# Kernel tuning notes

Measured on AMD Instinct MI355X. Metric: run time of the kernel, lower is better.

The kernel has to match this reference:

```python
import jax, jax.numpy as jnp
import numpy as np

SEQ, B, H, NP, HN = 2048, 2, 2048, 16, 128
SCALE = 1.0 / 11.313708498984761  # 1/sqrt(128), hardcoded in the source baddbmm


def setup_inputs() -> dict:
    key = jax.random.key(0)
    k1, k2, k3 = jax.random.split(key, 3)
    return {
        "hidden_states": jax.random.normal(k1, (SEQ, B, H), dtype=jnp.float32),
        "w_qkv": jax.random.normal(k2, (3 * H, H), dtype=jnp.float32) * 0.02,
        "w_out": jax.random.normal(k3, (H, H), dtype=jnp.float32) * 0.02,
    }


def reference(hidden_states, w_qkv, w_out):
    s, b, h = hidden_states.shape
    # QKV projection (column-parallel linear, no bias): [s, b, 3h]
    qkv = hidden_states @ w_qkv.T
    # [s, b, np, 3*hn] then split (num_query_groups == num_heads)
    qkv = qkv.reshape(s, b, NP, 3 * HN)
    q, k, v = qkv[..., :HN], qkv[..., HN:2 * HN], qkv[..., 2 * HN:]
    # baddbmm QK^T with alpha = 1/sqrt(128): scores [b, np, sq, sk]
    scores = jnp.einsum("sbnh,tbnh->bnst", q, k) * SCALE
    # scale_t == 1 then plain softmax (fallback path; no mask applied)
    prob = jax.nn.softmax(scores, axis=-1)
    # context: bmm(prob, V) -> [sq, b, np, hn] -> [sq, b, h]
    ctx = jnp.einsum("bnst,tbnh->sbnh", prob, v).reshape(s, b, h)
    # row-parallel output linear (no bias)
    return ctx @ w_out.T
```

## Files before the change

kernel.cpp:

```cpp
#include <hip/hip_runtime.h>
#include <stdint.h>

#define SEQ 2048
#define BATCH 2
#define HID 2048
#define NHEADS 16
#define HDIM 128
#define QKV_LD 6144
#define SCALE_F 0.08838834764831845f
#define LOG2E_F 1.4426950408889634f

typedef unsigned short u16;
using bf16x8 = __attribute__((ext_vector_type(8))) short;
using f32x4  = __attribute__((ext_vector_type(4))) float;

__device__ inline u16 f2bf(float f) {
  union { float f; uint32_t u; } c; c.f = f;
  uint32_t u = c.u;
  uint32_t r = (u + 0x7fffu + ((u >> 16) & 1u)) >> 16;
  return (u16)r;
}

__device__ inline void gl_lds16(const u16* g, u16* l) {
  __builtin_amdgcn_global_load_lds((const __attribute__((address_space(1))) void*)g,
                                   (__attribute__((address_space(3))) void*)l,
                                   16, 0, 0);
}

__global__ void cvt_all(const float* __restrict__ hs, const float* __restrict__ wqkv,
                        const float* __restrict__ wout, u16* __restrict__ ws_out) {
  int i = blockIdx.x * blockDim.x + threadIdx.x;
  const float* src;
  int j;
  float sc = 1.0f;
  if (i < 2097152) { src = hs; j = i; }
  else if (i < 5242880) {
    j = i - 2097152; src = wqkv;
    const int f = j >> 9;
    if ((f % 384) < 128) sc = SCALE_F;
  } else { j = i - 5242880; src = wout; }
  float4 v = ((const float4*)src)[j];
  ushort4 o;
  o.x = f2bf(v.x * sc); o.y = f2bf(v.y * sc); o.z = f2bf(v.z * sc); o.w = f2bf(v.w * sc);
  ((ushort4*)ws_out)[i] = o;
}

template<int MODE>
__global__ __launch_bounds__(256)
void gemm_bt(const u16* __restrict__ A, const u16* __restrict__ Bw,
             void* __restrict__ Cout, u16* __restrict__ vt, int M, int N, int K) {
  __shared__ __align__(16) u16 As[128 * 64];
  __shared__ __align__(16) u16 Bs[128 * 64];
  const int bm = blockIdx.x, bn = blockIdx.y;
  const int tid = threadIdx.x;
  const int wave = tid >> 6, lane = tid & 63;
  const int quad = lane >> 4, l16 = lane & 15;
  const int wm = (wave >> 1) * 64, wn = (wave & 1) * 64;
  f32x4 acc[4][4] = {};

  const u16* Ablk = A + (size_t)(bm * 128) * K;
  const u16* Bblk = Bw + (size_t)(bn * 128) * K;

  for (int k0 = 0; k0 < K; k0 += 64) {
    __syncthreads();
    #pragma unroll
    for (int p = 0; p < 4; ++p) {
      int j = p * 256 + tid;
      int r = j >> 3, cs = j & 7, c = cs ^ (r & 7);
      gl_lds16(Ablk + (size_t)r * K + k0 + c * 8, As + (p * 256 + wave * 64) * 8);
      gl_lds16(Bblk + (size_t)r * K + k0 + c * 8, Bs + (p * 256 + wave * 64) * 8);
    }
    __syncthreads();
    #pragma unroll
    for (int ks = 0; ks < 2; ++ks) {
      bf16x8 af[4], bfr[4];
      #pragma unroll
      for (int mt = 0; mt < 4; ++mt) {
        int row = wm + mt * 16 + l16;
        int cc = (ks * 4 + quad) ^ (row & 7);
        af[mt] = *(const bf16x8*)&As[(row * 8 + cc) * 8];
      }
      #pragma unroll
      for (int nt = 0; nt < 4; ++nt) {
        int row = wn + nt * 16 + l16;
        int cc = (ks * 4 + quad) ^ (row & 7);
        bfr[nt] = *(const bf16x8*)&Bs[(row * 8 + cc) * 8];
      }
      #pragma unroll
      for (int mt = 0; mt < 4; ++mt)
        #pragma unroll
        for (int nt = 0; nt < 4; ++nt)
          acc[mt][nt] = __builtin_amdgcn_mfma_f32_16x16x32_bf16(af[mt], bfr[nt], acc[mt][nt], 0, 0, 0);
    }
  }

  if (MODE == 1 && (bn % 3) == 2) {
    const int h = bn / 3;
    u16* vt0 = vt + ((size_t)h * HDIM) * SEQ;
    u16* vt1 = vt + ((size_t)(NHEADS + h) * HDIM) * SEQ;
    #pragma unroll
    for (int mt = 0; mt < 4; ++mt)
      #pragma unroll
      for (int nt = 0; nt < 4; ++nt) {
        const int hd = wn + nt * 16 + l16;
        const int s0 = (bm * 128 + wm + mt * 16 + quad * 4) >> 1;
        uint32_t w0 = (uint32_t)f2bf(acc[mt][nt][0]) | ((uint32_t)f2bf(acc[mt][nt][2]) << 16);
        uint32_t w1 = (uint32_t)f2bf(acc[mt][nt][1]) | ((uint32_t)f2bf(acc[mt][nt][3]) << 16);
        *(uint32_t*)&vt0[(size_t)hd * SEQ + s0] = w0;
        *(uint32_t*)&vt1[(size_t)hd * SEQ + s0] = w1;
      }
    return;
  }

  #pragma unroll
  for (int mt = 0; mt < 4; ++mt)
    #pragma unroll
    for (int nt = 0; nt < 4; ++nt)
      #pragma unroll
      for (int r = 0; r < 4; ++r) {
        int row = bm * 128 + wm + mt * 16 + quad * 4 + r;
        int col = bn * 128 + wn + nt * 16 + l16;
        float v = acc[mt][nt][r];
        if (MODE == 1) ((u16*)Cout)[(size_t)row * N + col] = f2bf(v);
        else           ((float*)Cout)[(size_t)row * N + col] = v;
      }
}

__global__ __launch_bounds__(512, 2)
void attn(const u16* __restrict__ qkv, const u16* __restrict__ vt_g, u16* __restrict__ ctx) {
  const int qt = blockIdx.x, head = blockIdx.y, b = blockIdx.z;
  const int q0 = qt * 256;
  __shared__ __align__(16) u16 Ks[2][64 * 128];
  __shared__ __align__(16) u16 Vt[2][144 * 64];
  __shared__ __align__(16) u16 PsT[256 * 64];
  const int tid = threadIdx.x;
  const int wave = tid >> 6, lane = tid & 63;
  const int quad = lane >> 4, l16 = lane & 15;

  const u16* qkv_bh = qkv + (size_t)b * QKV_LD + head * 384;
  const u16* vt = vt_g + (size_t)(b * NHEADS + head) * HDIM * SEQ;

  if (tid < 128) {
    const int row = 128 + (tid >> 3), c = tid & 7;
    const u16 v = (row == 128) ? (u16)0x3F80 : (u16)0;
    ushort4 q4; q4.x = v; q4.y = v; q4.z = v; q4.w = v;
    #pragma unroll
    for (int bb = 0; bb < 2; ++bb) {
      *(ushort4*)&Vt[bb][(row * 8 + c) * 8] = q4;
      *(ushort4*)&Vt[bb][(row * 8 + c) * 8 + 4] = q4;
    }
  }

  bf16x8 qf[2][4];
  #pragma unroll
  for (int h = 0; h < 4; ++h) {
    __syncthreads();
    #pragma unroll
    for (int p = 0; p < 2; ++p) {
      int j = p * 512 + tid;
      int r = j >> 4, cs = j & 15, c = cs ^ (r & 7);
      gl_lds16(qkv_bh + (size_t)(q0 + h * 64 + r) * (BATCH * QKV_LD) + c * 8,
               Ks[0] + (p * 512 + wave * 64) * 8);
    }
    __syncthreads();
    if ((wave >> 1) == h) {
      #pragma unroll
      for (int nt = 0; nt < 2; ++nt)
        #pragma unroll
        for (int ks = 0; ks < 4; ++ks) {
          int row = (wave & 1) * 32 + nt * 16 + l16;
          int cc = (ks * 4 + quad) ^ (row & 7);
          qf[nt][ks] = *(const bf16x8*)&Ks[0][(row * 16 + cc) * 8];
        }
    }
  }

  auto stageKV = [&](int kt, int bb) {
    #pragma unroll
    for (int p = 0; p < 2; ++p) {
      int j = p * 512 + tid;
      int r = j >> 4, cs = j & 15, c = cs ^ (r & 7);
      gl_lds16(qkv_bh + (size_t)(kt + r) * (BATCH * QKV_LD) + 128 + c * 8,
               Ks[bb] + (p * 512 + wave * 64) * 8);
    }
    #pragma unroll
    for (int p = 0; p < 2; ++p) {
      int j = p * 512 + tid;
      int hd = j >> 3, cs = j & 7, c = cs ^ (hd & 7);
      gl_lds16(vt + (size_t)hd * SEQ + kt + c * 8,
               Vt[bb] + (p * 512 + wave * 64) * 8);
    }
  };

  f32x4 ot[9][2] = {};

  __syncthreads();
  stageKV(0, 0);
  __syncthreads();

  for (int it = 0; it < SEQ / 64; ++it) {
    const int cur = it & 1;
    if (it + 1 < SEQ / 64) stageKV((it + 1) * 64, cur ^ 1);
    const u16* Kb = Ks[cur];
    const u16* Vb = Vt[cur];

    f32x4 st[4][2] = {};
    #pragma unroll
    for (int ks = 0; ks < 4; ++ks) {
      bf16x8 kf[4];
      #pragma unroll
      for (int mt = 0; mt < 4; ++mt) {
        int key = mt * 16 + l16;
        int cc = (ks * 4 + quad) ^ (key & 7);
        kf[mt] = *(const bf16x8*)&Kb[(key * 16 + cc) * 8];
      }
      __builtin_amdgcn_s_setprio(1);
      #pragma unroll
      for (int mt = 0; mt < 4; ++mt)
        #pragma unroll
        for (int nt = 0; nt < 2; ++nt)
          st[mt][nt] = __builtin_amdgcn_mfma_f32_16x16x32_bf16(kf[mt], qf[nt][ks], st[mt][nt], 0, 0, 0);
      __builtin_amdgcn_s_setprio(0);
    }

    #pragma unroll
    for (int mt = 0; mt < 4; ++mt)
      #pragma unroll
      for (int nt = 0; nt < 2; ++nt) {
        ushort4 pk;
        union { float f; uint32_t u; } cv;
        cv.f = __builtin_amdgcn_exp2f(st[mt][nt][0] * LOG2E_F); pk.x = (u16)(cv.u >> 16);
        cv.f = __builtin_amdgcn_exp2f(st[mt][nt][1] * LOG2E_F); pk.y = (u16)(cv.u >> 16);
        cv.f = __builtin_amdgcn_exp2f(st[mt][nt][2] * LOG2E_F); pk.z = (u16)(cv.u >> 16);
        cv.f = __builtin_amdgcn_exp2f(st[mt][nt][3] * LOG2E_F); pk.w = (u16)(cv.u >> 16);
        const int q = wave * 32 + nt * 16 + l16;
        const int kc = mt * 2 + (quad >> 1);
        *(ushort4*)&PsT[q * 64 + ((kc ^ (l16 & 7)) * 8 + (quad & 1) * 4)] = pk;
      }

    #pragma unroll
    for (int ks = 0; ks < 2; ++ks) {
      bf16x8 pf[2], vf[9];
      #pragma unroll
      for (int nt = 0; nt < 2; ++nt) {
        const int q = wave * 32 + nt * 16 + l16;
        const int cc = (ks * 4 + quad) ^ (l16 & 7);
        pf[nt] = *(const bf16x8*)&PsT[q * 64 + cc * 8];
      }
      #pragma unroll
      for (int mt = 0; mt < 9; ++mt) {
        const int hd = mt * 16 + l16;
        const int cc = (ks * 4 + quad) ^ (hd & 7);
        vf[mt] = *(const bf16x8*)&Vb[(hd * 8 + cc) * 8];
      }
      __builtin_amdgcn_s_setprio(1);
      #pragma unroll
      for (int mt = 0; mt < 9; ++mt)
        #pragma unroll
        for (int nt = 0; nt < 2; ++nt)
          ot[mt][nt] = __builtin_amdgcn_mfma_f32_16x16x32_bf16(vf[mt], pf[nt], ot[mt][nt], 0, 0, 0);
      __builtin_amdgcn_s_setprio(0);
    }

    __syncthreads();
  }

  #pragma unroll
  for (int nt = 0; nt < 2; ++nt) {
    const float lv = __shfl(ot[8][nt][0], l16);
    const float inv_l = 1.0f / lv;
    const int s = q0 + wave * 32 + nt * 16 + l16;
    u16* dst = ctx + ((size_t)s * BATCH + b) * HID + head * HDIM;
    #pragma unroll
    for (int mt = 0; mt < 8; ++mt) {
      ushort4 w;
      w.x = f2bf(ot[mt][nt][0] * inv_l);
      w.y = f2bf(ot[mt][nt][1] * inv_l);
      w.z = f2bf(ot[mt][nt][2] * inv_l);
      w.w = f2bf(ot[mt][nt][3] * inv_l);
      *(ushort4*)&dst[mt * 16 + quad * 4] = w;
    }
  }
}

extern "C" void kernel_launch(void* const* d_in, const int* in_sizes, int n_in,
                              void* d_out, int out_size, void* d_ws, size_t ws_size,
                              hipStream_t stream) {
  const float* hs   = (const float*)d_in[0];
  const float* wqkv = (const float*)d_in[1];
  const float* wout = (const float*)d_in[2];
  float* out = (float*)d_out;
  char* ws = (char*)d_ws;

  u16* hs_bf   = (u16*)(ws);
  u16* wqkv_bf = (u16*)(ws + 16777216);
  u16* wout_bf = (u16*)(ws + 41943040);
  u16* qkv_bf  = (u16*)(ws + 50331648);
  u16* vt_bf   = (u16*)(ws + 100663296);
  u16* ctx_bf  = hs_bf;

  cvt_all<<<24576, 256, 0, stream>>>(hs, wqkv, wout, (u16*)ws);

  gemm_bt<1><<<dim3(32, 48), 256, 0, stream>>>(hs_bf, wqkv_bf, qkv_bf, vt_bf, 4096, 6144, 2048);

  attn<<<dim3(8, NHEADS, BATCH), 512, 0, stream>>>(qkv_bf, vt_bf, ctx_bf);

  gemm_bt<0><<<dim3(32, 16), 256, 0, stream>>>(ctx_bf, wout_bf, out, nullptr, 4096, 2048, 2048);
}
```

Baseline: 365.1 us.

## Split output GEMM into 128x64 tiles and compute softmax denominator with VALU sums

The output projection gets its own kernel with 128x64 tiles, launching 1024 blocks instead of 512 so more CUs are kept busy on the 4096x2048 GEMM. In attention, the extra ones-row MFMA tile that produced the softmax row sum is removed. The denominator is instead accumulated from the bf16-rounded probabilities in registers and reduced with cross-lane shuffles. This cuts one ninth of the PV MFMAs and some LDS, in exchange for extra VALU adds and lower data reuse in the smaller output GEMM tiles.

```diff
diff --git a/kernel.cpp b/kernel.cpp
--- a/kernel.cpp
+++ b/kernel.cpp
@@ -45,10 +45,9 @@
   ((ushort4*)ws_out)[i] = o;
 }
 
-template<int MODE>
 __global__ __launch_bounds__(256)
 void gemm_bt(const u16* __restrict__ A, const u16* __restrict__ Bw,
-             void* __restrict__ Cout, u16* __restrict__ vt, int M, int N, int K) {
+             u16* __restrict__ Cout, u16* __restrict__ vt, int M, int N, int K) {
   __shared__ __align__(16) u16 As[128 * 64];
   __shared__ __align__(16) u16 Bs[128 * 64];
   const int bm = blockIdx.x, bn = blockIdx.y;
@@ -94,7 +93,7 @@
     }
   }
 
-  if (MODE == 1 && (bn % 3) == 2) {
+  if ((bn % 3) == 2) {
     const int h = bn / 3;
     u16* vt0 = vt + ((size_t)h * HDIM) * SEQ;
     u16* vt1 = vt + ((size_t)(NHEADS + h) * HDIM) * SEQ;
@@ -120,9 +119,72 @@
       for (int r = 0; r < 4; ++r) {
         int row = bm * 128 + wm + mt * 16 + quad * 4 + r;
         int col = bn * 128 + wn + nt * 16 + l16;
-        float v = acc[mt][nt][r];
-        if (MODE == 1) ((u16*)Cout)[(size_t)row * N + col] = f2bf(v);
-        else           ((float*)Cout)[(size_t)row * N + col] = v;
+        Cout[(size_t)row * N + col] = f2bf(acc[mt][nt][r]);
+      }
+}
+
+__global__ __launch_bounds__(256)
+void gemm_out(const u16* __restrict__ A, const u16* __restrict__ Bw,
+              float* __restrict__ Cout, int M, int N, int K) {
+  __shared__ __align__(16) u16 As[128 * 64];
+  __shared__ __align__(16) u16 Bs[64 * 64];
+  const int bm = blockIdx.x, bn = blockIdx.y;
+  const int tid = threadIdx.x;
+  const int wave = tid >> 6, lane = tid & 63;
+  const int quad = lane >> 4, l16 = lane & 15;
+  const int wm = (wave >> 1) * 64, wn = (wave & 1) * 32;
+  f32x4 acc[4][2] = {};
+
+  const u16* Ablk = A + (size_t)(bm * 128) * K;
+  const u16* Bblk = Bw + (size_t)(bn * 64) * K;
+
+  for (int k0 = 0; k0 < K; k0 += 64) {
+    __syncthreads();
+    #pragma unroll
+    for (int p = 0; p < 4; ++p) {
+      int j = p * 256 + tid;
+      int r = j >> 3, cs = j & 7, c = cs ^ (r & 7);
+      gl_lds16(Ablk + (size_t)r * K + k0 + c * 8, As + (p * 256 + wave * 64) * 8);
+    }
+    #pragma unroll
+    for (int p = 0; p < 2; ++p) {
+      int j = p * 256 + tid;
+      int r = j >> 3, cs = j & 7, c = cs ^ (r & 7);
+      gl_lds16(Bblk + (size_t)r * K + k0 + c * 8, Bs + (p * 256 + wave * 64) * 8);
+    }
+    __syncthreads();
+    #pragma unroll
+    for (int ks = 0; ks < 2; ++ks) {
+      bf16x8 af[4], bfr[2];
+      #pragma unroll
+      for (int mt = 0; mt < 4; ++mt) {
+        int row = wm + mt * 16 + l16;
+        int cc = (ks * 4 + quad) ^ (row & 7);
+        af[mt] = *(const bf16x8*)&As[(row * 8 + cc) * 8];
+      }
+      #pragma unroll
+      for (int nt = 0; nt < 2; ++nt) {
+        int row = wn + nt * 16 + l16;
+        int cc = (ks * 4 + quad) ^ (row & 7);
+        bfr[nt] = *(const bf16x8*)&Bs[(row * 8 + cc) * 8];
+      }
+      #pragma unroll
+      for (int mt = 0; mt < 4; ++mt)
+        #pragma unroll
+        for (int nt = 0; nt < 2; ++nt)
+          acc[mt][nt] = __builtin_amdgcn_mfma_f32_16x16x32_bf16(af[mt], bfr[nt], acc[mt][nt], 0, 0, 0);
+    }
+  }
+
+  #pragma unroll
+  for (int mt = 0; mt < 4; ++mt)
+    #pragma unroll
+    for (int nt = 0; nt < 2; ++nt)
+      #pragma unroll
+      for (int r = 0; r < 4; ++r) {
+        int row = bm * 128 + wm + mt * 16 + quad * 4 + r;
+        int col = bn * 64 + wn + nt * 16 + l16;
+        Cout[(size_t)row * N + col] = acc[mt][nt][r];
       }
 }
 
@@ -131,7 +193,7 @@
   const int qt = blockIdx.x, head = blockIdx.y, b = blockIdx.z;
   const int q0 = qt * 256;
   __shared__ __align__(16) u16 Ks[2][64 * 128];
-  __shared__ __align__(16) u16 Vt[2][144 * 64];
+  __shared__ __align__(16) u16 Vt[2][128 * 64];
   __shared__ __align__(16) u16 PsT[256 * 64];
   const int tid = threadIdx.x;
   const int wave = tid >> 6, lane = tid & 63;
@@ -139,17 +201,6 @@
 
   const u16* qkv_bh = qkv + (size_t)b * QKV_LD + head * 384;
   const u16* vt = vt_g + (size_t)(b * NHEADS + head) * HDIM * SEQ;
-
-  if (tid < 128) {
-    const int row = 128 + (tid >> 3), c = tid & 7;
-    const u16 v = (row == 128) ? (u16)0x3F80 : (u16)0;
-    ushort4 q4; q4.x = v; q4.y = v; q4.z = v; q4.w = v;
-    #pragma unroll
-    for (int bb = 0; bb < 2; ++bb) {
-      *(ushort4*)&Vt[bb][(row * 8 + c) * 8] = q4;
-      *(ushort4*)&Vt[bb][(row * 8 + c) * 8 + 4] = q4;
-    }
-  }
 
   bf16x8 qf[2][4];
   #pragma unroll
@@ -192,7 +243,8 @@
     }
   };
 
-  f32x4 ot[9][2] = {};
+  f32x4 ot[8][2] = {};
+  float lacc[2] = {0.0f, 0.0f};
 
   __syncthreads();
   stageKV(0, 0);
@@ -228,11 +280,15 @@
       #pragma unroll
       for (int nt = 0; nt < 2; ++nt) {
         ushort4 pk;
-        union { float f; uint32_t u; } cv;
+        union { float f; uint32_t u; } cv, rv;
         cv.f = __builtin_amdgcn_exp2f(st[mt][nt][0] * LOG2E_F); pk.x = (u16)(cv.u >> 16);
         cv.f = __builtin_amdgcn_exp2f(st[mt][nt][1] * LOG2E_F); pk.y = (u16)(cv.u >> 16);
         cv.f = __builtin_amdgcn_exp2f(st[mt][nt][2] * LOG2E_F); pk.z = (u16)(cv.u >> 16);
         cv.f = __builtin_amdgcn_exp2f(st[mt][nt][3] * LOG2E_F); pk.w = (u16)(cv.u >> 16);
+        rv.u = (uint32_t)pk.x << 16; lacc[nt] += rv.f;
+        rv.u = (uint32_t)pk.y << 16; lacc[nt] += rv.f;
+        rv.u = (uint32_t)pk.z << 16; lacc[nt] += rv.f;
+        rv.u = (uint32_t)pk.w << 16; lacc[nt] += rv.f;
         const int q = wave * 32 + nt * 16 + l16;
         const int kc = mt * 2 + (quad >> 1);
         *(ushort4*)&PsT[q * 64 + ((kc ^ (l16 & 7)) * 8 + (quad & 1) * 4)] = pk;
@@ -240,7 +296,7 @@
 
     #pragma unroll
     for (int ks = 0; ks < 2; ++ks) {
-      bf16x8 pf[2], vf[9];
+      bf16x8 pf[2], vf[8];
       #pragma unroll
       for (int nt = 0; nt < 2; ++nt) {
         const int q = wave * 32 + nt * 16 + l16;
@@ -248,14 +304,14 @@
         pf[nt] = *(const bf16x8*)&PsT[q * 64 + cc * 8];
       }
       #pragma unroll
-      for (int mt = 0; mt < 9; ++mt) {
+      for (int mt = 0; mt < 8; ++mt) {
         const int hd = mt * 16 + l16;
         const int cc = (ks * 4 + quad) ^ (hd & 7);
         vf[mt] = *(const bf16x8*)&Vb[(hd * 8 + cc) * 8];
       }
       __builtin_amdgcn_s_setprio(1);
       #pragma unroll
-      for (int mt = 0; mt < 9; ++mt)
+      for (int mt = 0; mt < 8; ++mt)
         #pragma unroll
         for (int nt = 0; nt < 2; ++nt)
           ot[mt][nt] = __builtin_amdgcn_mfma_f32_16x16x32_bf16(vf[mt], pf[nt], ot[mt][nt], 0, 0, 0);
@@ -267,7 +323,9 @@
 
   #pragma unroll
   for (int nt = 0; nt < 2; ++nt) {
-    const float lv = __shfl(ot[8][nt][0], l16);
+    float lv = lacc[nt];
+    lv += __shfl_xor(lv, 16);
+    lv += __shfl_xor(lv, 32);
     const float inv_l = 1.0f / lv;
     const int s = q0 + wave * 32 + nt * 16 + l16;
     u16* dst = ctx + ((size_t)s * BATCH + b) * HID + head * HDIM;
@@ -301,9 +359,9 @@
 
   cvt_all<<<24576, 256, 0, stream>>>(hs, wqkv, wout, (u16*)ws);
 
-  gemm_bt<1><<<dim3(32, 48), 256, 0, stream>>>(hs_bf, wqkv_bf, qkv_bf, vt_bf, 4096, 6144, 2048);
+  gemm_bt<<<dim3(32, 48), 256, 0, stream>>>(hs_bf, wqkv_bf, qkv_bf, vt_bf, 4096, 6144, 2048);
 
   attn<<<dim3(8, NHEADS, BATCH), 512, 0, stream>>>(qkv_bf, vt_bf, ctx_bf);
 
-  gemm_bt<0><<<dim3(32, 16), 256, 0, stream>>>(ctx_bf, wout_bf, out, nullptr, 4096, 2048, 2048);
-}
+  gemm_out<<<dim3(32, 32), 256, 0, stream>>>(ctx_bf, wout_bf, out, 4096, 2048, 2048);
+}
```

Result: no change. 367.6 us (+0.7%).
